# Kernel tuning notes

Measured on AMD Instinct MI355X. Metric: run time of the kernel, lower is better.

Reference implementation:

```python
import jax, jax.numpy as jnp
import numpy as np

LSTM = 256
NUM_CELLS = 5
BLOCKS = 6
TEMP = 5.0
TANH_C = 1.1


def setup_inputs() -> dict:
    key = jax.random.key(0)
    ks = jax.random.split(key, 8)
    s = 0.05  # small init so sigmoids/tanh stay in sane range
    return {
        "enc_w": jax.random.normal(ks[0], (5, LSTM), jnp.float32) * s,
        "w_ih": jax.random.normal(ks[1], (4 * LSTM, LSTM), jnp.float32) * s,
        "w_hh": jax.random.normal(ks[2], (4 * LSTM, LSTM), jnp.float32) * s,
        "b_ih": jax.random.normal(ks[3], (4 * LSTM,), jnp.float32) * s,
        "b_hh": jax.random.normal(ks[4], (4 * LSTM,), jnp.float32) * s,
        "w1": jax.random.normal(ks[5], (LSTM, LSTM), jnp.float32) * s,
        "w2": jax.random.normal(ks[6], (LSTM, LSTM), jnp.float32) * s,
        "v": jax.random.normal(ks[7], (LSTM,), jnp.float32) * s,
    }


def _lstm_cell(x, h, c, w_ih, w_hh, b_ih, b_hh):
    # torch.nn.LSTMCell gate order: i, f, g, o
    g = w_ih @ x + b_ih + w_hh @ h + b_hh  # [4*LSTM]
    i, f, gg, o = jnp.split(g, 4)
    i, f, o = jax.nn.sigmoid(i), jax.nn.sigmoid(f), jax.nn.sigmoid(o)
    c2 = f * c + i * jnp.tanh(gg)
    h2 = o * jnp.tanh(c2)
    return h2, c2


def _run_sampler(bkey, enc_w, w_ih, w_hh, b_ih, b_hh, w1, w2, v):
    zeros = jnp.zeros((LSTM,), jnp.float32)
    inputs = enc_w[0]  # encoder(0)
    anchors = []
    anchors_w1 = []
    prev_h = prev_c = zeros
    # first two layers: LSTM always fed zero state (faithful to source)
    for _ in range(2):
        prev_h, prev_c = _lstm_cell(inputs, zeros, zeros, w_ih, w_hh, b_ih, b_hh)
        anchors.append(zeros)
        anchors_w1.append(w1 @ prev_h)
    arc_seq, log_probs, entropies = [], [], []
    step = 0
    for layer_id in range(2, NUM_CELLS + 2):
        for _ in range(2):
            prev_h, prev_c = _lstm_cell(inputs, prev_h, prev_c, w_ih, w_hh, b_ih, b_hh)
            q = jnp.tanh(jnp.stack(anchors_w1[:layer_id]) + w2 @ prev_h)  # [layer_id, LSTM]
            logits = (q @ v) / TEMP  # [layer_id]
            logits = TANH_C * jnp.tanh(logits)
            skey = jax.random.fold_in(bkey, step); step += 1
            index = jax.random.categorical(skey, logits)
            lsm = jax.nn.log_softmax(logits)
            arc_seq.append(index)
            log_probs.append(-lsm[index])  # F.cross_entropy
            entropies.append(jax.lax.stop_gradient(-jnp.sum(lsm * jnp.exp(lsm))))
            inputs = jnp.stack(anchors[:layer_id])[index]
        prev_h, prev_c = _lstm_cell(inputs, prev_h, prev_c, w_ih, w_hh, b_ih, b_hh)
        anchors.append(prev_h)
        anchors_w1.append(w1 @ prev_h)
        inputs = enc_w[0]
    arc = jnp.stack(arc_seq)  # [2*NUM_CELLS] int
    return arc, sum(entropies), sum(log_probs), prev_c, prev_h


def reference(enc_w, w_ih, w_hh, b_ih, b_hh, w1, w2, v):
    key = jax.random.key(42)
    all_arc = []
    all_entropy = jnp.float32(0.0)
    all_log_prob = jnp.float32(0.0)
    c = h = None
    for b in range(BLOCKS):
        arc, ent, lp, c, h = _run_sampler(
            jax.random.fold_in(key, b), enc_w, w_ih, w_hh, b_ih, b_hh, w1, w2, v)
        all_arc.append(arc)
        all_entropy = all_entropy + ent
        all_log_prob = all_log_prob + lp
    return (jnp.stack(all_arc), all_log_prob, all_entropy, c[None, :], h[None, :])
```

## Files before the change

kernel.cpp:

```cpp
#include <hip/hip_runtime.h>
#include <stdint.h>


#define NBLK  6
#define PWG   8
#define THR   512
#define TINYF 1.17549435e-38f
#define HTAGB 0xC3B00000u
#define YTAGB 0xE1700000u
#define DONE_MAGIC 0x444f4e45

typedef unsigned long long u64;
struct U2 { uint32_t x, y; };

#define W_DONE 0u
#define W_PART 64u
#define W_HX   128u
#define W_YMB  24704u
#define W_NEED 221312u

#define S_READY 0u
#define S_DONE  192u
#define S_PART  224u
#define S_HP    320u
#define S_ACC   24896u
#define FXS     67108864.0f
#define READY_MAGIC 0x52454459

__device__ __forceinline__ U2 tf2x32(uint32_t k0, uint32_t k1,
                                     uint32_t c0, uint32_t c1) {
  uint32_t ks2 = k0 ^ k1 ^ 0x1BD11BDAu;
  uint32_t x0 = c0 + k0, x1 = c1 + k1;
#define TFR(r) { x0 += x1; x1 = (x1 << (r)) | (x1 >> (32 - (r))); x1 ^= x0; }
  TFR(13) TFR(15) TFR(26) TFR(6)   x0 += k1;  x1 += ks2 + 1u;
  TFR(17) TFR(29) TFR(16) TFR(24)  x0 += ks2; x1 += k0 + 2u;
  TFR(13) TFR(15) TFR(26) TFR(6)   x0 += k0;  x1 += k1 + 3u;
  TFR(17) TFR(29) TFR(16) TFR(24)  x0 += k1;  x1 += ks2 + 4u;
  TFR(13) TFR(15) TFR(26) TFR(6)   x0 += ks2; x1 += k0 + 5u;
#undef TFR
  U2 r; r.x = x0; r.y = x1; return r;
}

__device__ __forceinline__ float sigf(float x) {
  return 1.0f / (1.0f + expf(-x));
}
__device__ __forceinline__ void istore(int* p, int v) {
  __hip_atomic_store(p, v, __ATOMIC_RELAXED, __HIP_MEMORY_SCOPE_AGENT);
}
__device__ __forceinline__ int iload(const int* p) {
  return __hip_atomic_load(p, __ATOMIC_RELAXED, __HIP_MEMORY_SCOPE_AGENT);
}
__device__ __forceinline__ void hstore(u64* p, u64 v) {
  __hip_atomic_store(p, v, __ATOMIC_RELAXED, __HIP_MEMORY_SCOPE_AGENT);
}
__device__ __forceinline__ u64 hload(const u64* p) {
  return __hip_atomic_load(p, __ATOMIC_RELAXED, __HIP_MEMORY_SCOPE_AGENT);
}
__device__ __forceinline__ void fstore(float* p, float v) {
  __hip_atomic_store(p, v, __ATOMIC_RELAXED, __HIP_MEMORY_SCOPE_AGENT);
}
__device__ __forceinline__ float fload(const float* p) {
  return __hip_atomic_load(p, __ATOMIC_RELAXED, __HIP_MEMORY_SCOPE_AGENT);
}
__device__ __forceinline__ u64 pollw(const u64* p, uint32_t want) {
  u64 v;
  for (;;) {
    v = hload(p);
    if ((uint32_t)(v >> 32) == want) return v;
    __builtin_amdgcn_s_sleep(1);
  }
}

__global__ __launch_bounds__(THR, 2) void ctrl_v13(
    const float* __restrict__ enc_w,
    const float* __restrict__ wih,
    const float* __restrict__ whh,
    const float* __restrict__ b_ih,
    const float* __restrict__ b_hh,
    const float* __restrict__ w1,
    const float* __restrict__ w2,
    const float* __restrict__ vvec,
    unsigned char* __restrict__ ws,
    float* __restrict__ out) {

  const int b = blockIdx.x & 7;
  const int p = blockIdx.x >> 3;
  if (b >= NBLK) return;
  const int tid = threadIdx.x;

  int*   done = (int*)(ws + W_DONE);
  float* part = (float*)(ws + W_PART);
  u64*   hx   = (u64*)(ws + W_HX);
  u64*   ymb  = (u64*)(ws + W_YMB);

  const int rl = tid & 127, s = tid >> 7;
  const int grow = (rl >> 5) * 256 + p * 32 + (rl & 31);
  const int k0 = s * 64;
  const int rr = tid & 255, ks = tid >> 8;
  const int cb = p * 32 + ks * 16;

  __shared__ __align__(16) float gateL[THR];
  __shared__ __align__(16) float hL[256], encL[256], vL[256];
  __shared__ __align__(16) float anchL[4][256];
  __shared__ __align__(16) float w2hS[256], aw1S[6][256];
  __shared__ float rowSumL[128], biasS[128], h2S[32];
  __shared__ float logitL[8];
  __shared__ int   selL;

  if (tid < 256) { encL[tid] = enc_w[tid]; vL[tid] = vvec[tid]; }
  if (tid < 128) {
    int r = (tid >> 5) * 256 + p * 32 + (tid & 31);
    biasS[tid] = b_ih[r] + b_hh[r];
  }

  float4 wihr[16], whhr[16];
  #pragma unroll
  for (int c = 0; c < 16; ++c) {
    wihr[c] = *(const float4*)(wih + grow * 256 + k0 + c * 4);
    whhr[c] = *(const float4*)(whh + grow * 256 + k0 + c * 4);
  }
  float w1c[16], w2c[16];
  #pragma unroll
  for (int j = 0; j < 16; ++j) {
    w1c[j] = w1[rr * 256 + cb + j];
    w2c[j] = w2[rr * 256 + cb + j];
  }
  __syncthreads();

  auto dotIH = [&](const float* x) {
    float a = 0.0f;
    #pragma unroll
    for (int c = 0; c < 16; ++c) {
      float4 xv = *(const float4*)(x + k0 + c * 4);
      float4 w = wihr[c];
      a += w.x * xv.x + w.y * xv.y + w.z * xv.z + w.w * xv.w;
    }
    return a;
  };
  auto dotHH = [&]() {
    float a = 0.0f;
    #pragma unroll
    for (int c = 0; c < 16; ++c) {
      float4 xv = *(const float4*)(hL + k0 + c * 4);
      float4 w = whhr[c];
      a += w.x * xv.x + w.y * xv.y + w.z * xv.z + w.w * xv.w;
    }
    return a;
  };

  const float encih = dotIH(encL);

  float cv = 0.0f;
  U2 bk = tf2x32(0u, 42u, 0u, (uint32_t)b);
  int k = 1, step = 0;
  float lpAcc = 0.0f, entAcc = 0.0f;

  auto cell = [&](float gacc, int mode, int aid, int cid) {
    gateL[tid] = gacc;
    __syncthreads();
    if (tid < 128) {
      float ssum = 0.0f;
      #pragma unroll
      for (int j = 0; j < 4; ++j) ssum += gateL[j * 128 + tid];
      rowSumL[tid] = ssum + biasS[tid];
    }
    __syncthreads();
    if (tid < 32) {
      float gi = rowSumL[tid],       gf = rowSumL[32 + tid];
      float gg2 = rowSumL[64 + tid], go = rowSumL[96 + tid];
      float c2 = sigf(gf) * cv + sigf(gi) * tanhf(gg2);
      float h2 = sigf(go) * tanhf(c2);
      cv = c2;
      h2S[tid] = h2;
      if (mode == 2) {
        if (b == NBLK - 1) { out[62 + p * 32 + tid] = cv; out[318 + p * 32 + tid] = h2; }
      } else {
        hstore(&hx[(k & 1) * 1536 + b * 256 + p * 32 + tid],
               ((u64)(HTAGB | (uint32_t)k) << 32) | (u64)__float_as_uint(h2));
      }
    }
    __syncthreads();
    if (mode == 2) return;

    {
      const float* wc = (mode == 1) ? w1c : w2c;
      float yp = 0.0f;
      #pragma unroll
      for (int j = 0; j < 16; ++j) yp += wc[j] * h2S[ks * 16 + j];
      gateL[tid] = yp;
    }
    __syncthreads();

    const uint32_t wantY = YTAGB | (uint32_t)k;
    const uint32_t wantH = HTAGB | (uint32_t)k;
    u64* yslot = ymb + (size_t)(k & 1) * 12288 + (size_t)b * 2048;
    if (tid < 256) {
      float yp2 = gateL[tid] + gateL[256 + tid];
      hstore(yslot + p * 256 + tid,
             ((u64)wantY << 32) | (u64)__float_as_uint(yp2));
      u64 v = pollw(&hx[(k & 1) * 1536 + b * 256 + tid], wantH);
      float hv = __uint_as_float((uint32_t)v);
      hL[tid] = hv;
      if (mode == 1 && cid >= 0) anchL[cid][tid] = hv;
    } else {
      const int e = tid - 256;
      const u64* bp = yslot + e;
      float own = gateL[e] + gateL[256 + e];
      float ys[8];
      unsigned got = 1u << p;
      #pragma unroll
      for (int q = 0; q < 8; ++q) ys[q] = (q == p) ? own : 0.0f;
      for (;;) {
        bool all = true;
        #pragma unroll
        for (int q = 0; q < 8; ++q) {
          if (!(got & (1u << q))) {
            u64 w = hload(bp + q * 256);
            if ((uint32_t)(w >> 32) == wantY) {
              ys[q] = __uint_as_float((uint32_t)w);
              got |= 1u << q;
            } else {
              all = false;
            }
          }
        }
        if (all) break;
        __builtin_amdgcn_s_sleep(1);
      }
      float y = 0.0f;
      #pragma unroll
      for (int q = 0; q < 8; ++q) y += ys[q];
      if (mode == 1) aw1S[aid][e] = y; else w2hS[e] = y;
    }
    __syncthreads();
    ++k;
  };

  auto resolve = [&](int L) -> int {
    int wv = tid >> 6, lane = tid & 63;
    if (wv < L) {
      float a = 0.0f;
      #pragma unroll
      for (int j = 0; j < 4; ++j) {
        int kk = j * 64 + lane;
        a += tanhf(aw1S[wv][kk] + w2hS[kk]) * vL[kk];
      }
      a += __shfl_down(a, 32);
      a += __shfl_down(a, 16);
      a += __shfl_down(a, 8);
      a += __shfl_down(a, 4);
      a += __shfl_down(a, 2);
      a += __shfl_down(a, 1);
      if (lane == 0) logitL[wv] = a;
    }
    __syncthreads();
    if (tid < 64) {
      float lg = 0.0f, sgum = -1e30f;
      if (tid < L) {
        lg = 1.1f * tanhf(logitL[tid] * 0.2f);
        U2 sk = tf2x32(bk.x, bk.y, 0u, (uint32_t)step);
        U2 r2 = tf2x32(sk.x, sk.y, 0u, (uint32_t)tid);
        uint32_t bits = r2.x ^ r2.y;
        float u = __uint_as_float((bits >> 9) | 0x3f800000u) - 1.0f;
        u = fmaxf(TINYF, u + TINYF);
        sgum = lg - logf(-logf(u));
      }
      int bi = 0;
      float best = __shfl(sgum, 0, 64);
      for (int j = 1; j < L; ++j) {
        float sj = __shfl(sgum, j, 64);
        if (sj > best) { best = sj; bi = j; }
      }
      float mx = __shfl(lg, 0, 64);
      for (int j = 1; j < L; ++j) mx = fmaxf(mx, __shfl(lg, j, 64));
      float se = 0.0f;
      for (int j = 0; j < L; ++j) se += expf(__shfl(lg, j, 64) - mx);
      float lse = logf(se);
      float lgbi = __shfl(lg, bi, 64);
      float es = 0.0f;
      for (int j = 0; j < L; ++j) {
        float l = __shfl(lg, j, 64) - mx - lse;
        es += l * expf(l);
      }
      if (tid == 0) {
        lpAcc += -(lgbi - mx - lse);
        entAcc += -es;
        selL = bi;
        if (p == 0) out[b * 10 + step] = (float)bi;
      }
    }
    __syncthreads();
    step++;
    return selL;
  };

  cell(encih, 1, 0, -1);
  if (tid < 256) aw1S[1][tid] = aw1S[0][tid];
  __syncthreads();

  for (int L = 2; L <= 6; ++L) {
    { float hh = dotHH(); cell(encih + hh, 0, 0, -1); }
    {
      float hh = dotHH();
      int s1 = resolve(L);
      float a = (s1 >= 2) ? dotIH(&anchL[s1 - 2][0]) : 0.0f;
      cell(a + hh, 0, 0, -1);
    }
    {
      float hh = dotHH();
      int s2 = resolve(L);
      float a = (s2 >= 2) ? dotIH(&anchL[s2 - 2][0]) : 0.0f;
      if (L < 6) cell(a + hh, 1, L, L - 2);
      else       cell(a + hh, 2, 0, -1);
    }
  }

  if (p == 0 && tid == 0) {
    fstore(&part[2 * b], lpAcc);
    fstore(&part[2 * b + 1], entAcc);
    __builtin_amdgcn_s_waitcnt(0);
    istore(&done[b], DONE_MAGIC);
    if (b == NBLK - 1) {
      float lp = 0.0f, en = 0.0f;
      for (int j = 0; j < NBLK; ++j) {
        while (iload(&done[j]) != DONE_MAGIC) __builtin_amdgcn_s_sleep(1);
        lp += fload(&part[2 * j]);
        en += fload(&part[2 * j + 1]);
      }
      out[60] = lp;
      out[61] = en;
    }
  }
}

__global__ __launch_bounds__(1024) void ctrl_small(
    const float* __restrict__ enc_w,
    const float* __restrict__ wih,
    const float* __restrict__ whh,
    const float* __restrict__ b_ih,
    const float* __restrict__ b_hh,
    const float* __restrict__ w1,
    const float* __restrict__ w2,
    const float* __restrict__ vvec,
    unsigned char* __restrict__ ws,
    float* __restrict__ out) {

  const int b = blockIdx.x & 7;
  const int p = blockIdx.x >> 3;
  if (b >= NBLK) return;
  const int tid = threadIdx.x;

  int*   ready = (int*)(ws + S_READY);
  int*   done  = (int*)(ws + S_DONE);
  float* part  = (float*)(ws + S_PART);
  u64*   hp    = (u64*)(ws + S_HP);
  int*   acc   = (int*)(ws + S_ACC);

  const int rl = tid >> 3, s = tid & 7;
  const int g = rl >> 5, el = rl & 31;
  const int row = g * 256 + p * 32 + el;
  const int k0 = s * 32;
  const int rr = tid & 255, ks = tid >> 8;

  __shared__ __align__(16) float hL[256], encL[256], vL[256];
  __shared__ __align__(16) float anchL[4][256];
  __shared__ __align__(16) float partL[1024];
  __shared__ __align__(16) float w2hS[256], aw1S[6][256];
  __shared__ float rowSumL[128], biasS[128], h2S[32];
  __shared__ float logitL[8];
  __shared__ int   selL;

  if (tid < 256) { encL[tid] = enc_w[tid]; vL[tid] = vvec[tid]; }
  if (tid < 128) {
    int gg = tid >> 5, ee = tid & 31, r = gg * 256 + p * 32 + ee;
    biasS[tid] = b_ih[r] + b_hh[r];
  }

  float4 wihr[8], whhr[8];
  #pragma unroll
  for (int c = 0; c < 8; ++c) {
    int cc = (c + s) & 7;
    wihr[c] = *(const float4*)(wih + row * 256 + k0 + cc * 4);
    whhr[c] = *(const float4*)(whh + row * 256 + k0 + cc * 4);
  }
  float w1c[8], w2c[8];
  #pragma unroll
  for (int j = 0; j < 8; ++j) {
    w1c[j] = w1[rr * 256 + p * 32 + ks * 8 + j];
    w2c[j] = w2[rr * 256 + p * 32 + ks * 8 + j];
  }

  if (tid < 32) istore(&acc[1 * (NBLK * 256) + b * 256 + p * 32 + tid], 0);
  __syncthreads();
  if (tid == 0) istore(&ready[b * 8 + p], READY_MAGIC);
  if (tid < 8) {
    while (iload(&ready[b * 8 + tid]) != READY_MAGIC)
      __builtin_amdgcn_s_sleep(1);
  }
  __syncthreads();

  auto dotIH = [&](const float* x) {
    float a = 0.0f;
    #pragma unroll
    for (int c = 0; c < 8; ++c) {
      int cc = (c + s) & 7;
      float4 xv = *(const float4*)(x + k0 + cc * 4);
      float4 w = wihr[c];
      a += w.x * xv.x + w.y * xv.y + w.z * xv.z + w.w * xv.w;
    }
    return a;
  };
  auto dotHH = [&]() {
    float a = 0.0f;
    #pragma unroll
    for (int c = 0; c < 8; ++c) {
      int cc = (c + s) & 7;
      float4 xv = *(const float4*)(hL + k0 + cc * 4);
      float4 w = whhr[c];
      a += w.x * xv.x + w.y * xv.y + w.z * xv.z + w.w * xv.w;
    }
    return a;
  };

  const float encih = dotIH(encL);
  float cv = 0.0f;
  U2 bk = tf2x32(0u, 42u, 0u, (uint32_t)b);
  int k = 1, step = 0;
  float lpAcc = 0.0f, entAcc = 0.0f;

  auto cell = [&](float gacc, int mode, int aid, int cid) {
    partL[tid] = gacc;
    __syncthreads();
    if (tid < 128) {
      float ssum = 0.0f;
      #pragma unroll
      for (int j = 0; j < 8; ++j) ssum += partL[tid * 8 + j];
      rowSumL[tid] = ssum + biasS[tid];
    }
    __syncthreads();
    if (tid < 32) {
      float gi = rowSumL[tid],       gf = rowSumL[32 + tid];
      float gg2 = rowSumL[64 + tid], go = rowSumL[96 + tid];
      float c2 = sigf(gf) * cv + sigf(gi) * tanhf(gg2);
      float h2 = sigf(go) * tanhf(c2);
      cv = c2;
      h2S[tid] = h2;
      if (mode == 2 && b == NBLK - 1) {
        out[62 + p * 32 + tid] = cv;
        out[318 + p * 32 + tid] = h2;
      }
    }
    __syncthreads();
    if (mode == 2) return;
    {
      const float* wc = (mode == 1) ? w1c : w2c;
      float yp = 0.0f;
      #pragma unroll
      for (int j = 0; j < 8; ++j) yp += wc[j] * h2S[ks * 8 + j];
      atomicAdd(&acc[(k % 3) * (NBLK * 256) + b * 256 + rr],
                __float2int_rn(yp * FXS));
      if (tid < 32)
        istore(&acc[((k + 1) % 3) * (NBLK * 256) + b * 256 + p * 32 + tid], 0);
    }
    __syncthreads();
    if (tid < 32) {
      u64 pk = ((u64)(uint32_t)k << 32) | (u64)__float_as_uint(h2S[tid]);
      hstore(&hp[(k & 1) * (NBLK * 256) + b * 256 + p * 32 + tid], pk);
    }
    if (tid < 256) {
      u64 v;
      const u64* src = &hp[(k & 1) * (NBLK * 256) + b * 256 + tid];
      while ((int)(hload(src) >> 32) != k) __builtin_amdgcn_s_sleep(1);
      v = hload(src);
      float hv = __uint_as_float((uint32_t)v);
      hL[tid] = hv;
      if (mode == 1 && cid >= 0) anchL[cid][tid] = hv;
    }
    __syncthreads();
    if (tid < 256) {
      int iv = iload(&acc[(k % 3) * (NBLK * 256) + b * 256 + tid]);
      float f = (float)((double)iv * (1.0 / 67108864.0));
      if (mode == 1) aw1S[aid][tid] = f; else w2hS[tid] = f;
    }
    __syncthreads();
    ++k;
  };

  auto sample = [&](int L) -> int {
    int wv = tid >> 6, lane = tid & 63;
    if (wv < L) {
      float a = 0.0f;
      #pragma unroll
      for (int j = 0; j < 4; ++j) {
        int kk = lane * 4 + j;
        a += tanhf(aw1S[wv][kk] + w2hS[kk]) * vL[kk];
      }
      a += __shfl_down(a, 32);
      a += __shfl_down(a, 16);
      a += __shfl_down(a, 8);
      a += __shfl_down(a, 4);
      a += __shfl_down(a, 2);
      a += __shfl_down(a, 1);
      if (lane == 0) logitL[wv] = a;
    }
    __syncthreads();
    if (tid < 64) {
      float lg = 0.0f, sgum = -1e30f;
      if (tid < L) {
        lg = 1.1f * tanhf(logitL[tid] * 0.2f);
        U2 sk = tf2x32(bk.x, bk.y, 0u, (uint32_t)step);
        U2 r2 = tf2x32(sk.x, sk.y, 0u, (uint32_t)tid);
        uint32_t bits = r2.x ^ r2.y;
        float u = __uint_as_float((bits >> 9) | 0x3f800000u) - 1.0f;
        u = fmaxf(TINYF, u + TINYF);
        sgum = lg - logf(-logf(u));
      }
      int bi = 0;
      float best = __shfl(sgum, 0, 64);
      for (int j = 1; j < L; ++j) {
        float sj = __shfl(sgum, j, 64);
        if (sj > best) { best = sj; bi = j; }
      }
      float mx = __shfl(lg, 0, 64);
      for (int j = 1; j < L; ++j) mx = fmaxf(mx, __shfl(lg, j, 64));
      float se = 0.0f;
      for (int j = 0; j < L; ++j) se += expf(__shfl(lg, j, 64) - mx);
      float lse = logf(se);
      float lgbi = __shfl(lg, bi, 64);
      float es = 0.0f;
      for (int j = 0; j < L; ++j) {
        float l = __shfl(lg, j, 64) - mx - lse;
        es += l * expf(l);
      }
      if (tid == 0) {
        lpAcc += -(lgbi - mx - lse);
        entAcc += -es;
        selL = bi;
        if (p == 0) out[b * 10 + step] = (float)bi;
      }
    }
    __syncthreads();
    step++;
    return selL;
  };

  cell(encih, 1, 0, -1);
  if (tid < 256) aw1S[1][tid] = aw1S[0][tid];
  __syncthreads();
  for (int L = 2; L <= 6; ++L) {
    cell(encih + dotHH(), 0, 0, -1);
    int s1v = sample(L);
    {
      float a = (s1v >= 2) ? dotIH(&anchL[s1v - 2][0]) : 0.0f;
      cell(a + dotHH(), 0, 0, -1);
    }
    int s2v = sample(L);
    {
      float a = (s2v >= 2) ? dotIH(&anchL[s2v - 2][0]) : 0.0f;
      if (L < 6) cell(a + dotHH(), 1, L, L - 2);
      else       cell(a + dotHH(), 2, 0, -1);
    }
  }
  if (p == 0 && tid == 0) {
    fstore(&part[2 * b], lpAcc);
    fstore(&part[2 * b + 1], entAcc);
    __builtin_amdgcn_s_waitcnt(0);
    istore(&done[b], DONE_MAGIC);
    if (b == NBLK - 1) {
      float lp = 0.0f, en = 0.0f;
      for (int j = 0; j < NBLK; ++j) {
        while (iload(&done[j]) != DONE_MAGIC) __builtin_amdgcn_s_sleep(1);
        lp += fload(&part[2 * j]);
        en += fload(&part[2 * j + 1]);
      }
      out[60] = lp;
      out[61] = en;
    }
  }
}

extern "C" void kernel_launch(void* const* d_in, const int* in_sizes, int n_in,
                              void* d_out, int out_size, void* d_ws, size_t ws_size,
                              hipStream_t stream) {
  const float* enc = (const float*)d_in[0];
  const float* wih = (const float*)d_in[1];
  const float* whh = (const float*)d_in[2];
  const float* bih = (const float*)d_in[3];
  const float* bhh = (const float*)d_in[4];
  const float* w1  = (const float*)d_in[5];
  const float* w2  = (const float*)d_in[6];
  const float* v   = (const float*)d_in[7];
  unsigned char* ws = (unsigned char*)d_ws;
  float* out = (float*)d_out;

  if (ws_size >= W_NEED) {
    ctrl_v13<<<dim3(64), dim3(THR), 0, stream>>>(
        enc, wih, whh, bih, bhh, w1, w2, v, ws, out);
  } else {
    ctrl_small<<<dim3(64), dim3(1024), 0, stream>>>(
        enc, wih, whh, bih, bhh, w1, w2, v, ws, out);
  }
}
```

Measured before the change: 161.4 us.

## Use L2-scoped polling loads and contiguous per-element partial-sum slots for cross-workgroup exchange

Reworks the inter-workgroup handoff of hidden-state and projection partials. The partial-sum mailbox becomes element-major so each consumer thread reads all 8 producers' slots with one burst of contiguous loads. Polling uses inline-asm loads with the sc0 cache bit, falling back to the original agent-scope atomic loads after a budget of failed polls. Stores issue a plain store followed by the atomic store. The hand-written asm adds a risk of wrong cache coherence semantics on this chip, and the double store adds write traffic.

```diff
diff --git a/kernel.cpp b/kernel.cpp
--- a/kernel.cpp
+++ b/kernel.cpp
@@ -9,6 +9,7 @@
 #define HTAGB 0xC3B00000u
 #define YTAGB 0xE1700000u
 #define DONE_MAGIC 0x444f4e45
+#define FASTB 128
 
 typedef unsigned long long u64;
 struct U2 { uint32_t x, y; };
@@ -71,7 +72,42 @@
   }
 }
 
-__global__ __launch_bounds__(THR, 2) void ctrl_v13(
+__device__ __forceinline__ void dstore(u64* p, u64 v) {
+  asm volatile("global_store_dwordx2 %0, %1, off" :: "v"(p), "v"(v) : "memory");
+  __hip_atomic_store(p, v, __ATOMIC_RELAXED, __HIP_MEMORY_SCOPE_AGENT);
+}
+__device__ __forceinline__ u64 l2load(const u64* p) {
+  u64 v;
+  asm volatile("global_load_dwordx2 %0, %1, off sc0\n\t"
+               "s_waitcnt vmcnt(0)"
+               : "=&v"(v) : "v"(p) : "memory");
+  return v;
+}
+__device__ __forceinline__ void l2load8(const u64* p, u64* w) {
+  asm volatile(
+      "global_load_dwordx2 %0, %8, off sc0\n\t"
+      "global_load_dwordx2 %1, %8, off offset:8 sc0\n\t"
+      "global_load_dwordx2 %2, %8, off offset:16 sc0\n\t"
+      "global_load_dwordx2 %3, %8, off offset:24 sc0\n\t"
+      "global_load_dwordx2 %4, %8, off offset:32 sc0\n\t"
+      "global_load_dwordx2 %5, %8, off offset:40 sc0\n\t"
+      "global_load_dwordx2 %6, %8, off offset:48 sc0\n\t"
+      "global_load_dwordx2 %7, %8, off offset:56 sc0\n\t"
+      "s_waitcnt vmcnt(0)"
+      : "=&v"(w[0]), "=&v"(w[1]), "=&v"(w[2]), "=&v"(w[3]),
+        "=&v"(w[4]), "=&v"(w[5]), "=&v"(w[6]), "=&v"(w[7])
+      : "v"(p) : "memory");
+}
+__device__ __forceinline__ u64 pollf(const u64* p, uint32_t want, int& bud) {
+  for (;;) {
+    u64 v = (bud > 0) ? l2load(p) : hload(p);
+    if ((uint32_t)(v >> 32) == want) { if (bud > 0) bud = FASTB; return v; }
+    if (bud > 0) --bud;
+    __builtin_amdgcn_s_sleep(1);
+  }
+}
+
+__global__ __launch_bounds__(THR, 2) void ctrl_v14(
     const float* __restrict__ enc_w,
     const float* __restrict__ wih,
     const float* __restrict__ whh,
@@ -154,6 +190,7 @@
   U2 bk = tf2x32(0u, 42u, 0u, (uint32_t)b);
   int k = 1, step = 0;
   float lpAcc = 0.0f, entAcc = 0.0f;
+  int fastB = FASTB;
 
   auto cell = [&](float gacc, int mode, int aid, int cid) {
     gateL[tid] = gacc;
@@ -175,7 +212,7 @@
       if (mode == 2) {
         if (b == NBLK - 1) { out[62 + p * 32 + tid] = cv; out[318 + p * 32 + tid] = h2; }
       } else {
-        hstore(&hx[(k & 1) * 1536 + b * 256 + p * 32 + tid],
+        dstore(&hx[(k & 1) * 1536 + b * 256 + p * 32 + tid],
                ((u64)(HTAGB | (uint32_t)k) << 32) | (u64)__float_as_uint(h2));
       }
     }
@@ -193,43 +230,37 @@
 
     const uint32_t wantY = YTAGB | (uint32_t)k;
     const uint32_t wantH = HTAGB | (uint32_t)k;
-    u64* yslot = ymb + (size_t)(k & 1) * 12288 + (size_t)b * 2048;
+    u64* ybase = ymb + (size_t)(k & 1) * 12288 + (size_t)b * 2048;
     if (tid < 256) {
       float yp2 = gateL[tid] + gateL[256 + tid];
-      hstore(yslot + p * 256 + tid,
+      dstore(ybase + (size_t)tid * 8 + p,
              ((u64)wantY << 32) | (u64)__float_as_uint(yp2));
-      u64 v = pollw(&hx[(k & 1) * 1536 + b * 256 + tid], wantH);
+      u64 v = pollf(&hx[(k & 1) * 1536 + b * 256 + tid], wantH, fastB);
       float hv = __uint_as_float((uint32_t)v);
       hL[tid] = hv;
       if (mode == 1 && cid >= 0) anchL[cid][tid] = hv;
     } else {
       const int e = tid - 256;
-      const u64* bp = yslot + e;
-      float own = gateL[e] + gateL[256 + e];
-      float ys[8];
-      unsigned got = 1u << p;
-      #pragma unroll
-      for (int q = 0; q < 8; ++q) ys[q] = (q == p) ? own : 0.0f;
+      const u64* bp8 = ybase + (size_t)e * 8;
+      u64 w[8];
       for (;;) {
-        bool all = true;
+        if (fastB > 0) {
+          l2load8(bp8, w);
+        } else {
+          #pragma unroll
+          for (int q = 0; q < 8; ++q) w[q] = hload(bp8 + q);
+        }
+        bool ok = true;
         #pragma unroll
-        for (int q = 0; q < 8; ++q) {
-          if (!(got & (1u << q))) {
-            u64 w = hload(bp + q * 256);
-            if ((uint32_t)(w >> 32) == wantY) {
-              ys[q] = __uint_as_float((uint32_t)w);
-              got |= 1u << q;
-            } else {
-              all = false;
-            }
-          }
-        }
-        if (all) break;
+        for (int q = 0; q < 8; ++q)
+          ok &= ((uint32_t)(w[q] >> 32) == wantY);
+        if (ok) { if (fastB > 0) fastB = FASTB; break; }
+        if (fastB > 0) --fastB;
         __builtin_amdgcn_s_sleep(1);
       }
       float y = 0.0f;
       #pragma unroll
-      for (int q = 0; q < 8; ++q) y += ys[q];
+      for (int q = 0; q < 8; ++q) y += __uint_as_float((uint32_t)w[q]);
       if (mode == 1) aw1S[aid][e] = y; else w2hS[e] = y;
     }
     __syncthreads();
@@ -594,7 +625,7 @@
   float* out = (float*)d_out;
 
   if (ws_size >= W_NEED) {
-    ctrl_v13<<<dim3(64), dim3(THR), 0, stream>>>(
+    ctrl_v14<<<dim3(64), dim3(THR), 0, stream>>>(
         enc, wih, whh, bih, bhh, w1, w2, v, ws, out);
   } else {
     ctrl_small<<<dim3(64), dim3(1024), 0, stream>>>(
```

Result: slower. 298.9 us (+85.1%).

## Centralize sampling decision in partition 0 and broadcast selected index

Applied to the files above, without the earlier changes.

Only workgroup partition p==0 now gathers the eight partial w1/w2 projections and runs the attention/sampling resolve step. It publishes the selected index through a tagged workspace slot that the other seven partitions poll. Partition 0 resolves before its hidden-state dot product, while the others overlap that dot product with waiting. This removes redundant all-to-all gathers and duplicated resolve work, at the cost of an extra cross-workgroup handoff on the critical path.

```diff
diff --git a/kernel.cpp b/kernel.cpp
--- a/kernel.cpp
+++ b/kernel.cpp
@@ -8,16 +8,18 @@
 #define TINYF 1.17549435e-38f
 #define HTAGB 0xC3B00000u
 #define YTAGB 0xE1700000u
+#define ITAGB 0xA5D00000u
 #define DONE_MAGIC 0x444f4e45
 
 typedef unsigned long long u64;
 struct U2 { uint32_t x, y; };
 
 #define W_DONE 0u
-#define W_PART 64u
-#define W_HX   128u
-#define W_YMB  24704u
-#define W_NEED 221312u
+#define W_PART 32u
+#define W_IDX  80u
+#define W_HX   320u
+#define W_YMB  24896u
+#define W_NEED 221504u
 
 #define S_READY 0u
 #define S_DONE  192u
@@ -71,7 +73,7 @@
   }
 }
 
-__global__ __launch_bounds__(THR, 2) void ctrl_v13(
+__global__ __launch_bounds__(THR, 2) void ctrl_v16(
     const float* __restrict__ enc_w,
     const float* __restrict__ wih,
     const float* __restrict__ whh,
@@ -90,6 +92,7 @@
 
   int*   done = (int*)(ws + W_DONE);
   float* part = (float*)(ws + W_PART);
+  int*   idxw = (int*)(ws + W_IDX);
   u64*   hx   = (u64*)(ws + W_HX);
   u64*   ymb  = (u64*)(ws + W_YMB);
 
@@ -193,43 +196,31 @@
 
     const uint32_t wantY = YTAGB | (uint32_t)k;
     const uint32_t wantH = HTAGB | (uint32_t)k;
-    u64* yslot = ymb + (size_t)(k & 1) * 12288 + (size_t)b * 2048;
+    u64* ybase = ymb + (size_t)(k & 1) * 12288 + (size_t)b * 2048;
     if (tid < 256) {
       float yp2 = gateL[tid] + gateL[256 + tid];
-      hstore(yslot + p * 256 + tid,
+      hstore(ybase + (size_t)p * 256 + tid,
              ((u64)wantY << 32) | (u64)__float_as_uint(yp2));
       u64 v = pollw(&hx[(k & 1) * 1536 + b * 256 + tid], wantH);
       float hv = __uint_as_float((uint32_t)v);
       hL[tid] = hv;
       if (mode == 1 && cid >= 0) anchL[cid][tid] = hv;
-    } else {
+    } else if (p == 0) {
       const int e = tid - 256;
-      const u64* bp = yslot + e;
-      float own = gateL[e] + gateL[256 + e];
-      float ys[8];
-      unsigned got = 1u << p;
-      #pragma unroll
-      for (int q = 0; q < 8; ++q) ys[q] = (q == p) ? own : 0.0f;
+      const u64* bp = ybase + e;
+      u64 w[8];
       for (;;) {
-        bool all = true;
         #pragma unroll
-        for (int q = 0; q < 8; ++q) {
-          if (!(got & (1u << q))) {
-            u64 w = hload(bp + q * 256);
-            if ((uint32_t)(w >> 32) == wantY) {
-              ys[q] = __uint_as_float((uint32_t)w);
-              got |= 1u << q;
-            } else {
-              all = false;
-            }
-          }
-        }
-        if (all) break;
+        for (int q = 0; q < 8; ++q) w[q] = hload(bp + q * 256);
+        uint32_t bad = 0u;
+        #pragma unroll
+        for (int q = 0; q < 8; ++q) bad |= ((uint32_t)(w[q] >> 32) ^ wantY);
+        if (bad == 0u) break;
         __builtin_amdgcn_s_sleep(1);
       }
       float y = 0.0f;
       #pragma unroll
-      for (int q = 0; q < 8; ++q) y += ys[q];
+      for (int q = 0; q < 8; ++q) y += __uint_as_float((uint32_t)w[q]);
       if (mode == 1) aw1S[aid][e] = y; else w2hS[e] = y;
     }
     __syncthreads();
@@ -237,78 +228,96 @@
   };
 
   auto resolve = [&](int L) -> int {
-    int wv = tid >> 6, lane = tid & 63;
-    if (wv < L) {
-      float a = 0.0f;
-      #pragma unroll
-      for (int j = 0; j < 4; ++j) {
-        int kk = j * 64 + lane;
-        a += tanhf(aw1S[wv][kk] + w2hS[kk]) * vL[kk];
-      }
-      a += __shfl_down(a, 32);
-      a += __shfl_down(a, 16);
-      a += __shfl_down(a, 8);
-      a += __shfl_down(a, 4);
-      a += __shfl_down(a, 2);
-      a += __shfl_down(a, 1);
-      if (lane == 0) logitL[wv] = a;
-    }
-    __syncthreads();
-    if (tid < 64) {
-      float lg = 0.0f, sgum = -1e30f;
-      if (tid < L) {
-        lg = 1.1f * tanhf(logitL[tid] * 0.2f);
-        U2 sk = tf2x32(bk.x, bk.y, 0u, (uint32_t)step);
-        U2 r2 = tf2x32(sk.x, sk.y, 0u, (uint32_t)tid);
-        uint32_t bits = r2.x ^ r2.y;
-        float u = __uint_as_float((bits >> 9) | 0x3f800000u) - 1.0f;
-        u = fmaxf(TINYF, u + TINYF);
-        sgum = lg - logf(-logf(u));
-      }
-      int bi = 0;
-      float best = __shfl(sgum, 0, 64);
-      for (int j = 1; j < L; ++j) {
-        float sj = __shfl(sgum, j, 64);
-        if (sj > best) { best = sj; bi = j; }
-      }
-      float mx = __shfl(lg, 0, 64);
-      for (int j = 1; j < L; ++j) mx = fmaxf(mx, __shfl(lg, j, 64));
-      float se = 0.0f;
-      for (int j = 0; j < L; ++j) se += expf(__shfl(lg, j, 64) - mx);
-      float lse = logf(se);
-      float lgbi = __shfl(lg, bi, 64);
-      float es = 0.0f;
-      for (int j = 0; j < L; ++j) {
-        float l = __shfl(lg, j, 64) - mx - lse;
-        es += l * expf(l);
-      }
+    if (p == 0) {
+      int wv = tid >> 6, lane = tid & 63;
+      if (wv < L) {
+        float a = 0.0f;
+        #pragma unroll
+        for (int j = 0; j < 4; ++j) {
+          int kk = j * 64 + lane;
+          a += tanhf(aw1S[wv][kk] + w2hS[kk]) * vL[kk];
+        }
+        a += __shfl_down(a, 32);
+        a += __shfl_down(a, 16);
+        a += __shfl_down(a, 8);
+        a += __shfl_down(a, 4);
+        a += __shfl_down(a, 2);
+        a += __shfl_down(a, 1);
+        if (lane == 0) logitL[wv] = a;
+      }
+      __syncthreads();
+      if (tid < 64) {
+        float lg = 0.0f, sgum = -1e30f;
+        if (tid < L) {
+          lg = 1.1f * tanhf(logitL[tid] * 0.2f);
+          U2 sk = tf2x32(bk.x, bk.y, 0u, (uint32_t)step);
+          U2 r2 = tf2x32(sk.x, sk.y, 0u, (uint32_t)tid);
+          uint32_t bits = r2.x ^ r2.y;
+          float u = __uint_as_float((bits >> 9) | 0x3f800000u) - 1.0f;
+          u = fmaxf(TINYF, u + TINYF);
+          sgum = lg - logf(-logf(u));
+        }
+        int bi = 0;
+        float best = __shfl(sgum, 0, 64);
+        for (int j = 1; j < L; ++j) {
+          float sj = __shfl(sgum, j, 64);
+          if (sj > best) { best = sj; bi = j; }
+        }
+        float mx = __shfl(lg, 0, 64);
+        for (int j = 1; j < L; ++j) mx = fmaxf(mx, __shfl(lg, j, 64));
+        float se = 0.0f;
+        for (int j = 0; j < L; ++j) se += expf(__shfl(lg, j, 64) - mx);
+        float lse = logf(se);
+        float lgbi = __shfl(lg, bi, 64);
+        float es = 0.0f;
+        for (int j = 0; j < L; ++j) {
+          float l = __shfl(lg, j, 64) - mx - lse;
+          es += l * expf(l);
+        }
+        if (tid == 0) {
+          lpAcc += -(lgbi - mx - lse);
+          entAcc += -es;
+          selL = bi;
+          out[b * 10 + step] = (float)bi;
+          istore(&idxw[b * 10 + step],
+                 (int)(ITAGB | ((uint32_t)step << 4) | (uint32_t)bi));
+        }
+      }
+      __syncthreads();
+    } else {
       if (tid == 0) {
-        lpAcc += -(lgbi - mx - lse);
-        entAcc += -es;
-        selL = bi;
-        if (p == 0) out[b * 10 + step] = (float)bi;
-      }
-    }
-    __syncthreads();
+        const uint32_t want = ITAGB | ((uint32_t)step << 4);
+        for (;;) {
+          uint32_t v = (uint32_t)iload(&idxw[b * 10 + step]);
+          if ((v & 0xFFFFFFF0u) == want) { selL = (int)(v & 15u); break; }
+          __builtin_amdgcn_s_sleep(1);
+        }
+      }
+      __syncthreads();
+    }
     step++;
     return selL;
   };
 
   cell(encih, 1, 0, -1);
-  if (tid < 256) aw1S[1][tid] = aw1S[0][tid];
-  __syncthreads();
+  if (p == 0) {
+    if (tid < 256) aw1S[1][tid] = aw1S[0][tid];
+    __syncthreads();
+  }
 
   for (int L = 2; L <= 6; ++L) {
     { float hh = dotHH(); cell(encih + hh, 0, 0, -1); }
     {
-      float hh = dotHH();
-      int s1 = resolve(L);
+      int s1; float hh;
+      if (p == 0) { s1 = resolve(L); hh = dotHH(); }
+      else        { hh = dotHH(); s1 = resolve(L); }
       float a = (s1 >= 2) ? dotIH(&anchL[s1 - 2][0]) : 0.0f;
       cell(a + hh, 0, 0, -1);
     }
     {
-      float hh = dotHH();
-      int s2 = resolve(L);
+      int s2; float hh;
+      if (p == 0) { s2 = resolve(L); hh = dotHH(); }
+      else        { hh = dotHH(); s2 = resolve(L); }
       float a = (s2 >= 2) ? dotIH(&anchL[s2 - 2][0]) : 0.0f;
       if (L < 6) cell(a + hh, 1, L, L - 2);
       else       cell(a + hh, 2, 0, -1);
@@ -594,7 +603,7 @@
   float* out = (float*)d_out;
 
   if (ws_size >= W_NEED) {
-    ctrl_v13<<<dim3(64), dim3(THR), 0, stream>>>(
+    ctrl_v16<<<dim3(64), dim3(THR), 0, stream>>>(
         enc, wih, whh, bih, bhh, w1, w2, v, ws, out);
   } else {
     ctrl_small<<<dim3(64), dim3(1024), 0, stream>>>(
```

Measured after the change: 149.2 us. 7.6% less time.
